# Performance work log

Measured on AMD Instinct MI355X. Metric: run time of the kernel, lower is better.

## Reference

```python
import jax, jax.numpy as jnp
from jax import lax
import numpy as np

IN_CH, OUT_CH, K, STRIDE = 4, 256, 16, 8
D_STATE, D_CONV, EXPAND, HEADDIM = 128, 4, 2, 64
D_INNER = EXPAND * OUT_CH            # 512
NHEADS = D_INNER // HEADDIM          # 8
CONV_DIM = D_INNER + 2 * D_STATE     # 768 (ngroups=1)
D_IN_PROJ = 2 * D_INNER + 2 * D_STATE + NHEADS  # 1288
B_SZ, L = 8, 16384


def _conv1d(x, w, b, stride, padding):
    y = lax.conv_general_dilated(x, w, (stride,), padding,
                                 dimension_numbers=('NCH', 'OIH', 'NCH'))
    return y + b[None, :, None]


def _mamba2(u, in_proj_w, conv1d_w, conv1d_b, dt_bias, A_log, D_skip, norm_w, out_proj_w):
    # u: (b, l, d_model). Faithful Mamba2 forward (ngroups=1, rmsnorm gated, no biases on projections).
    b, l, _ = u.shape
    zxbcdt = jnp.einsum('bld,ed->ble', u, in_proj_w)           # (b, l, d_in_proj)
    z = zxbcdt[..., :D_INNER]
    xBC = zxbcdt[..., D_INNER:D_INNER + CONV_DIM]
    dt = jax.nn.softplus(zxbcdt[..., D_INNER + CONV_DIM:] + dt_bias)  # (b, l, h)
    # causal depthwise conv (torch pads d_conv-1 both sides then truncates to :l == left-pad only) + SiLU
    xBC = lax.conv_general_dilated(xBC.transpose(0, 2, 1), conv1d_w, (1,),
                                   [(D_CONV - 1, 0)], feature_group_count=CONV_DIM,
                                   dimension_numbers=('NCH', 'OIH', 'NCH'))
    xBC = jax.nn.silu((xBC + conv1d_b[None, :, None]).transpose(0, 2, 1))  # (b, l, conv_dim)
    xs = xBC[..., :D_INNER].reshape(b, l, NHEADS, HEADDIM)
    Bm = xBC[..., D_INNER:D_INNER + D_STATE]                   # (b, l, n)
    Cm = xBC[..., D_INNER + D_STATE:]                          # (b, l, n)
    A = -jnp.exp(A_log)                                        # (h,), scalar A per head
    dA = jnp.exp(dt * A)                                       # (b, l, h)

    def step(h, inp):
        dA_t, dt_t, x_t, B_t, C_t = inp
        h = h * dA_t[:, :, None, None] + jnp.einsum('bh,bhp,bn->bhpn', dt_t, x_t, B_t)
        return h, jnp.einsum('bhpn,bn->bhp', h, C_t)

    h0 = jnp.zeros((b, NHEADS, HEADDIM, D_STATE), dtype=u.dtype)
    _, ys = lax.scan(step, h0, (dA.swapaxes(0, 1), dt.swapaxes(0, 1),
                                xs.swapaxes(0, 1), Bm.swapaxes(0, 1), Cm.swapaxes(0, 1)))
    y = ys.swapaxes(0, 1) + D_skip[None, None, :, None] * xs   # (b, l, h, p)
    y = y.reshape(b, l, D_INNER) * jax.nn.silu(z)              # gated RMSNorm (norm_before_gate=False)
    y = y * lax.rsqrt(jnp.mean(y * y, axis=-1, keepdims=True) + 1e-5) * norm_w
    return jnp.einsum('ble,de->bld', y, out_proj_w)


def _forward(x, conv_w, conv_b, in_proj_w, conv1d_w, conv1d_b, dt_bias, A_log,
             D_skip, norm_w, out_proj_w, conv1_w, conv1_b, convT_w, convT_b):
    h = jax.nn.relu(_conv1d(x, conv_w, conv_b, STRIDE, 'VALID'))       # (b, out_ch, l')
    y = _mamba2(h.transpose(0, 2, 1), in_proj_w, conv1d_w, conv1d_b,
                dt_bias, A_log, D_skip, norm_w, out_proj_w)
    y = y.transpose(0, 2, 1)                                           # (b, out_ch, l')
    y = _conv1d(y, conv1_w, conv1_b, 1, [(7, 8)])  # torch padding='same', even kernel: left=7, right=8
    # ConvTranspose1d: torch weight (Cin, Cout, K) -> flipped OIH kernel + lhs dilation
    kern = jnp.flip(convT_w, -1).transpose(1, 0, 2)
    y = lax.conv_general_dilated(y, kern, (1,), [(K - 1, K - 1)], lhs_dilation=(STRIDE,),
                                 dimension_numbers=('NCH', 'OIH', 'NCH'))
    return y + convT_b[None, :, None]


def setup_inputs() -> dict:
    key = jax.random.key(0)
    ks = jax.random.split(key, 16)
    n = lambda k, shp, sc=0.05: jax.random.normal(k, shp, dtype=jnp.float32) * sc
    return {
        'x': jax.random.normal(ks[0], (B_SZ, IN_CH, L), dtype=jnp.float32),
        'conv_w': n(ks[1], (OUT_CH, IN_CH, K)),
        'conv_b': n(ks[2], (OUT_CH,)),
        'in_proj_w': n(ks[3], (D_IN_PROJ, OUT_CH)),
        'conv1d_w': n(ks[4], (CONV_DIM, 1, D_CONV), 0.3),
        'conv1d_b': n(ks[5], (CONV_DIM,), 0.1),
        'dt_bias': n(ks[6], (NHEADS,), 0.5),
        'A_log': jnp.log(jax.random.uniform(ks[7], (NHEADS,), minval=1.0, maxval=16.0)),
        'D_skip': n(ks[8], (NHEADS,), 1.0),
        'norm_w': jnp.ones((D_INNER,), dtype=jnp.float32),
        'out_proj_w': n(ks[9], (OUT_CH, D_INNER)),
        'conv1_w': n(ks[10], (STRIDE, OUT_CH, K)),
        'conv1_b': n(ks[11], (STRIDE,)),
        'convT_w': n(ks[12], (STRIDE, IN_CH, K)),
        'convT_b': n(ks[13], (IN_CH,)),
    }


def reference(x, conv_w, conv_b, in_proj_w, conv1d_w, conv1d_b, dt_bias, A_log,
              D_skip, norm_w, out_proj_w, conv1_w, conv1_b, convT_w, convT_b):
    return _forward(x, conv_w, conv_b, in_proj_w, conv1d_w, conv1d_b, dt_bias, A_log,
                    D_skip, norm_w, out_proj_w, conv1_w, conv1_b, convT_w, convT_b)
```

## Files before the change

kernel.cpp:

```cpp
#include <hip/hip_runtime.h>
#include <cstddef>
#include <cstdint>

constexpr int L_IN   = 16384;
constexpr int L_SEQ  = 2047;
constexpr int BATCH  = 8;
constexpr int M_TOK  = BATCH * L_SEQ;
constexpr int D_INNER = 512;
constexpr int NHEADS  = 8;
constexpr int HEADDIM = 64;
constexpr int D_STATE = 128;
constexpr int CONV_DIM = 768;
constexpr int D_IN_PROJ = 1288;

constexpr int QC  = 64;
constexpr int NCH = 32;

constexpr int TP = 84;

constexpr size_t OFF_U    = 0;
constexpr size_t OFF_PB   = OFF_U   + 2096128;
constexpr size_t OFF_ZB   = OFF_U   + 4192256;
constexpr size_t OFF_XBC  = OFF_ZB  + 4192256;
constexpr size_t OFF_DT   = OFF_XBC + 6288384;
constexpr size_t OFF_AW   = OFF_DT  + 131008;
constexpr size_t OFF_XC   = OFF_AW  + 131008;
constexpr size_t OFF_Y    = OFF_XC  + 6288384;
constexpr size_t OFF_YC1  = OFF_Y   + 4192256;
constexpr size_t OFF_PBUF = OFF_YC1 + 131008;
constexpr size_t OFF_HS   = OFF_PBUF + 2048;
constexpr size_t OFF_WBIN = OFF_HS  + 8388608;
constexpr size_t OFF_WBF  = OFF_WBIN + 164864;
constexpr size_t OFF_W2   = OFF_WBF + 8192;

using short8 = __attribute__((ext_vector_type(8))) short;
using short4v = __attribute__((ext_vector_type(4))) short;
using f32x4  = __attribute__((ext_vector_type(4))) float;
typedef unsigned short ushort_t;

__device__ __forceinline__ ushort_t f2bf(float f) {
  uint32_t u = __float_as_uint(f);
  u += 0x7fffu + ((u >> 16) & 1u);
  return (ushort_t)(u >> 16);
}
__device__ __forceinline__ float bf2f(ushort_t h) {
  return __uint_as_float(((uint32_t)h) << 16);
}
__device__ __forceinline__ float siluf(float a) { return a / (1.f + expf(-a)); }
__device__ __forceinline__ short8 ld8(const short* p) {
  short4v a = *(const short4v*)p;
  short4v b = *(const short4v*)(p + 4);
  short8 r;
  r[0] = a[0]; r[1] = a[1]; r[2] = a[2]; r[3] = a[3];
  r[4] = b[0]; r[5] = b[1]; r[6] = b[2]; r[7] = b[3];
  return r;
}
#define MFMA16(a, b, c) __builtin_amdgcn_mfma_f32_16x16x32_bf16(a, b, c, 0, 0, 0)

#define GLD_LDS(gp, lp) __builtin_amdgcn_global_load_lds( \
    (const __attribute__((address_space(1))) void*)(gp),  \
    (__attribute__((address_space(3))) void*)(lp), 16, 0, 0)

__global__ __launch_bounds__(256) void k_prep(const float* __restrict__ x,
    const float* __restrict__ w1, const float* __restrict__ w3,
    const float* __restrict__ conv1_w, const float* __restrict__ wout,
    ushort_t* __restrict__ PB, ushort_t* __restrict__ o1, ushort_t* __restrict__ o3,
    ushort_t* __restrict__ W2b) {
  const int bid = blockIdx.x;
  const int tid = threadIdx.x;
  if (bid < 512) {
    int idx = bid * 256 + tid;
    if (idx >= M_TOK * 8) return;
    int oct = idx & 7, row = idx >> 3;
    int t = row % L_SEQ, b = row / L_SEQ;
    int ic = oct >> 1, k0 = (oct & 1) * 8;
    const float* src = x + ((size_t)b * 4 + ic) * L_IN + t * 8 + k0;
    float4 a0 = *(const float4*)src;
    float4 a1 = *(const float4*)(src + 4);
    short8 o;
    o[0] = (short)f2bf(a0.x); o[1] = (short)f2bf(a0.y);
    o[2] = (short)f2bf(a0.z); o[3] = (short)f2bf(a0.w);
    o[4] = (short)f2bf(a1.x); o[5] = (short)f2bf(a1.y);
    o[6] = (short)f2bf(a1.z); o[7] = (short)f2bf(a1.w);
    *(short8*)(PB + (size_t)row * 64 + oct * 8) = o;
  } else if (bid < 1800) {
    int i = (bid - 512) * 256 + tid;
    if (i < D_IN_PROJ * 256) o1[i] = f2bf(w1[i]);
    if (i < 256 * 64)        o3[i] = f2bf(w3[i]);
  } else {
    const int r = bid - 1800;
    const int oc = r >> 4, k = r & 15;
    const int d0 = tid;
    float acc0 = 0.f, acc1 = 0.f;
    for (int o = 0; o < 256; o++) {
      float wv = conv1_w[((size_t)oc * 256 + o) * 16 + k];
      acc0 = fmaf(wv, wout[(size_t)o * 512 + d0], acc0);
      acc1 = fmaf(wv, wout[(size_t)o * 512 + d0 + 256], acc1);
    }
    W2b[(size_t)r * 512 + d0]       = f2bf(acc0);
    W2b[(size_t)r * 512 + d0 + 256] = f2bf(acc1);
  }
}

template<int EPI>
__global__ __launch_bounds__(256) void gemm_bf16(const ushort_t* __restrict__ A, int lda,
    const ushort_t* __restrict__ B, int ldb, float* __restrict__ C,
    const float* __restrict__ bias, int M, int N, int K, int nx,
    ushort_t* __restrict__ zb, ushort_t* __restrict__ xbcb,
    float* __restrict__ dtb, float* __restrict__ awb,
    const float* __restrict__ dt_bias, const float* __restrict__ A_log) {
  __shared__ __attribute__((aligned(16))) ushort_t sA[2][128 * 64];
  __shared__ __attribute__((aligned(16))) ushort_t sB[2][128 * 64];
  const int tid = threadIdx.x;
  const int cpx = gridDim.x >> 3;
  const int swz = (blockIdx.x & 7) * cpx + (blockIdx.x >> 3);
  const int m0 = (swz / nx) * 128, n0 = (swz % nx) * 128;
  const int w = tid >> 6, lane = tid & 63;
  const int l15 = lane & 15, lK = lane >> 4;
  const int wr = w >> 1, wc = w & 1;
  f32x4 acc[4][4] = {};

  auto STAGE = [&](int buf, int k0) {
#pragma unroll
    for (int j = 0; j < 4; j++) {
      int idx = j * 256 + tid;
      int r = idx >> 3;
      int ss = (idx & 7) ^ (r & 7);
      GLD_LDS(A + (size_t)(m0 + r) * lda + k0 + ss * 8, &sA[buf][(j * 256 + w * 64) * 8]);
      GLD_LDS(B + (size_t)(n0 + r) * ldb + k0 + ss * 8, &sB[buf][(j * 256 + w * 64) * 8]);
    }
  };

  STAGE(0, 0);
  __syncthreads();
  int cur = 0;
  for (int k0 = 0; k0 < K; k0 += 64) {
    if (k0 + 64 < K) STAGE(cur ^ 1, k0 + 64);
#pragma unroll
    for (int kk = 0; kk < 2; kk++) {
      short8 af[4], bf[4];
#pragma unroll
      for (int mt = 0; mt < 4; mt++) {
        int r = wr * 64 + mt * 16 + l15;
        af[mt] = *(const short8*)&sA[cur][r * 64 + (((kk * 4 + lK) ^ (r & 7)) * 8)];
      }
#pragma unroll
      for (int nt = 0; nt < 4; nt++) {
        int r = wc * 64 + nt * 16 + l15;
        bf[nt] = *(const short8*)&sB[cur][r * 64 + (((kk * 4 + lK) ^ (r & 7)) * 8)];
      }
#pragma unroll
      for (int mt = 0; mt < 4; mt++)
#pragma unroll
        for (int nt = 0; nt < 4; nt++)
          acc[mt][nt] = MFMA16(af[mt], bf[nt], acc[mt][nt]);
    }
    __syncthreads();
    cur ^= 1;
  }
  if constexpr (EPI == 1) {
    ushort_t* Cb = (ushort_t*)C;
#pragma unroll
    for (int mt = 0; mt < 4; mt++)
#pragma unroll
      for (int i = 0; i < 4; i++) {
        int gm = m0 + wr * 64 + mt * 16 + lK * 4 + i;
#pragma unroll
        for (int nt = 0; nt < 4; nt++) {
          int gn = n0 + wc * 64 + nt * 16 + l15;
          float v = fmaxf(acc[mt][nt][i] + bias[gn], 0.f);
          uint32_t mine = f2bf(v);
          uint32_t other = (uint32_t)__shfl_xor((int)mine, 1, 64);
          if (((lane & 1) == 0) && gm < M)
            *(uint32_t*)(Cb + (size_t)gm * N + gn) = mine | (other << 16);
        }
      }
  } else if constexpr (EPI == 3) {
    ushort_t* Cb = (ushort_t*)C;
#pragma unroll
    for (int mt = 0; mt < 4; mt++)
#pragma unroll
      for (int i = 0; i < 4; i++) {
        int gm = m0 + wr * 64 + mt * 16 + lK * 4 + i;
#pragma unroll
        for (int nt = 0; nt < 4; nt++) {
          int gn = n0 + wc * 64 + nt * 16 + l15;
          uint32_t mine = f2bf(acc[mt][nt][i]);
          uint32_t other = (uint32_t)__shfl_xor((int)mine, 1, 64);
          if (((lane & 1) == 0) && gm < M)
            *(uint32_t*)(Cb + (size_t)gm * N + gn) = mine | (other << 16);
        }
      }
  } else {
    if (n0 < 1280) {
      ushort_t* dst = (n0 < 512) ? zb : xbcb;
      const int ldd  = (n0 < 512) ? 512 : 768;
      const int coff = (n0 < 512) ? 0 : 512;
#pragma unroll
      for (int mt = 0; mt < 4; mt++)
#pragma unroll
        for (int i = 0; i < 4; i++) {
          int gm = m0 + wr * 64 + mt * 16 + lK * 4 + i;
#pragma unroll
          for (int nt = 0; nt < 4; nt++) {
            int gn = n0 + wc * 64 + nt * 16 + l15;
            uint32_t mine = f2bf(acc[mt][nt][i]);
            uint32_t other = (uint32_t)__shfl_xor((int)mine, 1, 64);
            if (((lane & 1) == 0) && gm < M)
              *(uint32_t*)(dst + (size_t)gm * ldd + (gn - coff)) = mine | (other << 16);
          }
        }
    } else {
#pragma unroll
      for (int mt = 0; mt < 4; mt++)
#pragma unroll
        for (int i = 0; i < 4; i++) {
          int gm = m0 + wr * 64 + mt * 16 + lK * 4 + i;
          if (gm >= M) continue;
#pragma unroll
          for (int nt = 0; nt < 4; nt++) {
            int gn = n0 + wc * 64 + nt * 16 + l15;
            if (gn < N) {
              int hd = gn - 1280;
              float v = acc[mt][nt][i] + dt_bias[hd];
              float sp = (v > 20.f) ? v : log1pf(expf(v));
              dtb[(size_t)gm * 8 + hd] = sp;
              awb[(size_t)gm * 8 + hd] = -expf(A_log[hd]) * sp;
            }
          }
        }
    }
  }
}

__global__ __launch_bounds__(192) void k_dw(const ushort_t* __restrict__ xbcb,
    const float* __restrict__ w, const float* __restrict__ bias,
    ushort_t* __restrict__ xcb) {
  const int bid = blockIdx.x;
  const int tb = bid & 511, b = bid >> 9;
  const int t0 = tb * 4;
  const int c = threadIdx.x * 4;
  const size_t rowb = (size_t)b * L_SEQ;
  float wr[4][4];
#pragma unroll
  for (int j = 0; j < 4; j++)
#pragma unroll
    for (int k = 0; k < 4; k++) wr[j][k] = w[(c + j) * 4 + k];
  const float4 bs = {bias[c], bias[c + 1], bias[c + 2], bias[c + 3]};
  float v[7][4];
#pragma unroll
  for (int r = 0; r < 7; r++) {
    int tt = t0 - 3 + r;
    if (tt >= 0 && tt < L_SEQ) {
      uint2 pk = *(const uint2*)(xbcb + (rowb + tt) * CONV_DIM + c);
      v[r][0] = bf2f((ushort_t)(pk.x & 0xffff));
      v[r][1] = bf2f((ushort_t)(pk.x >> 16));
      v[r][2] = bf2f((ushort_t)(pk.y & 0xffff));
      v[r][3] = bf2f((ushort_t)(pk.y >> 16));
    } else {
      v[r][0] = v[r][1] = v[r][2] = v[r][3] = 0.f;
    }
  }
#pragma unroll
  for (int o = 0; o < 4; o++) {
    int t = t0 + o;
    if (t >= L_SEQ) break;
    float a0 = bs.x, a1 = bs.y, a2 = bs.z, a3 = bs.w;
#pragma unroll
    for (int k = 0; k < 4; k++) {
      a0 = fmaf(v[o + k][0], wr[0][k], a0);
      a1 = fmaf(v[o + k][1], wr[1][k], a1);
      a2 = fmaf(v[o + k][2], wr[2][k], a2);
      a3 = fmaf(v[o + k][3], wr[3][k], a3);
    }
    uint2 ov;
    ov.x = (uint32_t)f2bf(siluf(a0)) | ((uint32_t)f2bf(siluf(a1)) << 16);
    ov.y = (uint32_t)f2bf(siluf(a2)) | ((uint32_t)f2bf(siluf(a3)) << 16);
    *(uint2*)(xcb + (rowb + t) * CONV_DIM + c) = ov;
  }
}

__global__ __launch_bounds__(256) void k_ssd_state(const ushort_t* __restrict__ xcb,
    const float* __restrict__ dtb, const float* __restrict__ aw,
    ushort_t* __restrict__ HSb, float* __restrict__ Pbuf) {
  const int L = (blockIdx.x & 7) * 256 + (blockIdx.x >> 3);
  const int ch = L & 31, bh = L >> 5;
  const int b = bh >> 3, h = bh & 7;
  const int t0 = ch * QC;
  const int valid = (L_SEQ - t0 < QC) ? (L_SEQ - t0) : QC;
  const size_t rowbase = (size_t)b * L_SEQ;
  __shared__ __attribute__((aligned(16))) short sBT[128][TP];
  __shared__ __attribute__((aligned(16))) short sXw[64][TP];
  __shared__ float sW[64];
  __shared__ float sLtot;
  const int tid = threadIdx.x;
  if (tid < 64) {
    float aa = 0.f, dd = 0.f;
    if (tid < valid) { size_t r8 = (rowbase + t0 + tid) * 8 + h; aa = aw[r8]; dd = dtb[r8]; }
    float s = aa;
#pragma unroll
    for (int d = 1; d < 64; d <<= 1) { float o = __shfl_up(s, d, 64); if (tid >= d) s += o; }
    float Lt = __shfl(s, 63, 64);
    sW[tid] = expf(Lt - s) * dd;
    if (tid == 63) sLtot = s;
  }
  __syncthreads();
  for (int i = tid; i < 64 * 16; i += 256) {
    int r = i >> 4, q = (i & 15) * 8;
    short8 v = {0, 0, 0, 0, 0, 0, 0, 0};
    if (r < valid) v = *(const short8*)(xcb + (rowbase + t0 + r) * CONV_DIM + 512 + q);
#pragma unroll
    for (int j = 0; j < 8; j++) sBT[q + j][r] = v[j];
  }
  for (int i = tid; i < 64 * 8; i += 256) {
    int r = i >> 3, q = (i & 7) * 8;
    short8 v = {0, 0, 0, 0, 0, 0, 0, 0};
    if (r < valid) v = *(const short8*)(xcb + (rowbase + t0 + r) * CONV_DIM + h * 64 + q);
    float wv = sW[r];
#pragma unroll
    for (int j = 0; j < 8; j++) sXw[q + j][r] = (short)f2bf(bf2f((ushort_t)v[j]) * wv);
  }
  __syncthreads();
  const int w = tid >> 6, l15 = tid & 15, lK = (tid & 63) >> 4;
  f32x4 acc[2][4] = {};
  short8 afr[2][2];
#pragma unroll
  for (int j = 0; j < 2; j++)
#pragma unroll
    for (int kt = 0; kt < 2; kt++)
      afr[j][kt] = ld8(&sBT[(w * 2 + j) * 16 + l15][kt * 32 + lK * 8]);
#pragma unroll
  for (int pt = 0; pt < 4; pt++) {
#pragma unroll
    for (int kt = 0; kt < 2; kt++) {
      short8 bfr = ld8(&sXw[pt * 16 + l15][kt * 32 + lK * 8]);
      acc[0][pt] = MFMA16(afr[0][kt], bfr, acc[0][pt]);
      acc[1][pt] = MFMA16(afr[1][kt], bfr, acc[1][pt]);
    }
  }
  ushort_t* dst = HSb + ((size_t)bh * NCH + ch) * 8192;
#pragma unroll
  for (int j = 0; j < 2; j++)
#pragma unroll
    for (int pt = 0; pt < 4; pt++)
#pragma unroll
      for (int i = 0; i < 4; i++) {
        int n = (w * 2 + j) * 16 + lK * 4 + i, p = pt * 16 + l15;
        uint32_t mine = f2bf(acc[j][pt][i]);
        uint32_t other = (uint32_t)__shfl_xor((int)mine, 1, 64);
        if ((l15 & 1) == 0)
          *(uint32_t*)(dst + n * 64 + p) = mine | (other << 16);
      }
  if (tid == 0) Pbuf[bh * NCH + ch] = expf(sLtot);
}

__global__ __launch_bounds__(256) void k_ssd_comb(ushort_t* __restrict__ HSb,
                                                  const float* __restrict__ Pbuf) {
  const int bh = blockIdx.y;
  const int e2 = blockIdx.x * 256 + threadIdx.x;
  const size_t base = (size_t)bh * NCH * 8192 + (size_t)e2 * 2;
  uint32_t pk[NCH];
  float P[NCH];
#pragma unroll
  for (int c = 0; c < NCH; c++) pk[c] = *(const uint32_t*)(HSb + base + (size_t)c * 8192);
#pragma unroll
  for (int c = 0; c < NCH; c++) P[c] = Pbuf[bh * NCH + c];
  float run0 = 0.f, run1 = 0.f;
#pragma unroll
  for (int c = 0; c < NCH; c++) {
    run0 = fmaf(P[c], run0, bf2f((ushort_t)(pk[c] & 0xffff)));
    run1 = fmaf(P[c], run1, bf2f((ushort_t)(pk[c] >> 16)));
    pk[c] = (uint32_t)f2bf(run0) | ((uint32_t)f2bf(run1) << 16);
  }
#pragma unroll
  for (int c = 0; c < NCH; c++) *(uint32_t*)(HSb + base + (size_t)c * 8192) = pk[c];
}

__global__ __launch_bounds__(256) void k_ssd_y(const ushort_t* __restrict__ xcb,
    const float* __restrict__ dtb, const float* __restrict__ aw,
    const float* __restrict__ Dskip, const ushort_t* __restrict__ HSb,
    ushort_t* __restrict__ y16) {
  const int L = (blockIdx.x & 7) * 256 + (blockIdx.x >> 3);
  const int ch = L & 31, bh = L >> 5;
  const int b = bh >> 3, h = bh & 7;
  const int t0 = ch * QC;
  const int valid = (L_SEQ - t0 < QC) ? (L_SEQ - t0) : QC;
  const size_t rowbase = (size_t)b * L_SEQ;
  __shared__ __attribute__((aligned(16))) short sB[64][136];
  __shared__ __attribute__((aligned(16))) short sC[64][136];
  __shared__ __attribute__((aligned(16))) short sH[64][140];
  __shared__ __attribute__((aligned(16))) short sX[64][TP];
  __shared__ float sLrel[64], sdt[64], sEL[64];
  short (*sM)[72] = (short(*)[72])&sB[0][0];
  const int tid = threadIdx.x;
  if (tid < 64) {
    float aa = 0.f, dd = 0.f;
    if (tid < valid) { size_t r8 = (rowbase + t0 + tid) * 8 + h; aa = aw[r8]; dd = dtb[r8]; }
    float s = aa;
#pragma unroll
    for (int d = 1; d < 64; d <<= 1) { float o = __shfl_up(s, d, 64); if (tid >= d) s += o; }
    sLrel[tid] = s; sdt[tid] = dd; sEL[tid] = expf(s);
  }
  for (int i = tid; i < 64 * 16; i += 256) {
    int r = i >> 4, q = (i & 15) * 8;
    short8 vb = {0, 0, 0, 0, 0, 0, 0, 0}, vc = {0, 0, 0, 0, 0, 0, 0, 0};
    if (r < valid) {
      const ushort_t* rp = xcb + (rowbase + t0 + r) * CONV_DIM;
      vb = *(const short8*)(rp + 512 + q);
      vc = *(const short8*)(rp + 640 + q);
    }
    *(short8*)&sB[r][q] = vb;
    *(short8*)&sC[r][q] = vc;
  }
  for (int i = tid; i < 64 * 8; i += 256) {
    int r = i >> 3, q = (i & 7) * 8;
    short8 v = {0, 0, 0, 0, 0, 0, 0, 0};
    if (r < valid) v = *(const short8*)(xcb + (rowbase + t0 + r) * CONV_DIM + h * 64 + q);
#pragma unroll
    for (int j = 0; j < 8; j++) sX[q + j][r] = v[j];
  }
  for (int i = tid; i < 128 * 8; i += 256) {
    int n = i >> 3, q = (i & 7) * 8;
    short8 v = {0, 0, 0, 0, 0, 0, 0, 0};
    if (ch > 0) v = *(const short8*)(HSb + ((size_t)bh * NCH + (ch - 1)) * 8192 + n * 64 + q);
#pragma unroll
    for (int j = 0; j < 8; j++) sH[q + j][n] = v[j];
  }
  __syncthreads();
  const int w = tid >> 6, l15 = tid & 15, lK = (tid & 63) >> 4;
  short8 aC[4];
#pragma unroll
  for (int kt = 0; kt < 4; kt++)
    aC[kt] = *(const short8*)&sC[w * 16 + l15][kt * 32 + lK * 8];
  f32x4 g[4] = {};
#pragma unroll
  for (int st = 0; st < 4; st++)
#pragma unroll
    for (int kt = 0; kt < 4; kt++)
      g[st] = MFMA16(aC[kt], *(const short8*)&sB[st * 16 + l15][kt * 32 + lK * 8], g[st]);
  __syncthreads();
#pragma unroll
  for (int st = 0; st < 4; st++)
#pragma unroll
    for (int i = 0; i < 4; i++) {
      int tt = w * 16 + lK * 4 + i, ss = st * 16 + l15;
      float f = (ss <= tt) ? expf(sLrel[tt] - sLrel[ss]) * sdt[ss] : 0.f;
      sM[tt][ss] = (short)f2bf(g[st][i] * f);
    }
  __syncthreads();
  f32x4 acc[4] = {};
#pragma unroll
  for (int pt = 0; pt < 4; pt++)
#pragma unroll
    for (int kt = 0; kt < 4; kt++)
      acc[pt] = MFMA16(aC[kt], ld8(&sH[pt * 16 + l15][kt * 32 + lK * 8]), acc[pt]);
#pragma unroll
  for (int pt = 0; pt < 4; pt++)
#pragma unroll
    for (int i = 0; i < 4; i++)
      acc[pt][i] *= sEL[w * 16 + lK * 4 + i];
  short8 aM[2];
#pragma unroll
  for (int kt = 0; kt < 2; kt++)
    aM[kt] = *(const short8*)&sM[w * 16 + l15][kt * 32 + lK * 8];
#pragma unroll
  for (int pt = 0; pt < 4; pt++)
#pragma unroll
    for (int kt = 0; kt < 2; kt++)
      acc[pt] = MFMA16(aM[kt], ld8(&sX[pt * 16 + l15][kt * 32 + lK * 8]), acc[pt]);
  const float Dsk = Dskip[h];
#pragma unroll
  for (int pt = 0; pt < 4; pt++)
#pragma unroll
    for (int i = 0; i < 4; i++) {
      int tt = w * 16 + lK * 4 + i;
      int pp = pt * 16 + l15;
      float v = acc[pt][i] + Dsk * bf2f((ushort_t)sX[pp][tt]);
      uint32_t mine = f2bf(v);
      uint32_t other = (uint32_t)__shfl_xor((int)mine, 1, 64);
      if (((l15 & 1) == 0) && tt < valid)
        *(uint32_t*)(y16 + (rowbase + t0 + tt) * D_INNER + h * 64 + pp) = mine | (other << 16);
    }
}

__global__ __launch_bounds__(256) void k_norm(ushort_t* __restrict__ y16,
    const ushort_t* __restrict__ zb, const float* __restrict__ norm_w) {
  const int row = blockIdx.x * 4 + (threadIdx.x >> 6);
  const int lane = threadIdx.x & 63;
  const int c0 = lane * 8;
  ushort_t* yrow = y16 + (size_t)row * D_INNER;
  short8 yv = *(const short8*)(yrow + c0);
  short8 zv = *(const short8*)(zb + (size_t)row * 512 + c0);
  float v[8];
  float ss = 0.f;
#pragma unroll
  for (int j = 0; j < 8; j++) {
    float z = bf2f((ushort_t)zv[j]);
    float g = z / (1.f + expf(-z));
    v[j] = bf2f((ushort_t)yv[j]) * g;
    ss += v[j] * v[j];
  }
#pragma unroll
  for (int m = 32; m >= 1; m >>= 1) ss += __shfl_xor(ss, m, 64);
  float scale = rsqrtf(ss * (1.f / 512.f) + 1e-5f);
  float4 nw0 = *(const float4*)(norm_w + c0);
  float4 nw1 = *(const float4*)(norm_w + c0 + 4);
  short8 o;
  o[0] = (short)f2bf(v[0] * scale * nw0.x); o[1] = (short)f2bf(v[1] * scale * nw0.y);
  o[2] = (short)f2bf(v[2] * scale * nw0.z); o[3] = (short)f2bf(v[3] * scale * nw0.w);
  o[4] = (short)f2bf(v[4] * scale * nw1.x); o[5] = (short)f2bf(v[5] * scale * nw1.y);
  o[6] = (short)f2bf(v[6] * scale * nw1.z); o[7] = (short)f2bf(v[7] * scale * nw1.w);
  *(short8*)(yrow + c0) = o;
}

__global__ __launch_bounds__(256) void k_tail(const ushort_t* __restrict__ Yg,
    const float* __restrict__ b1, const float* __restrict__ wT,
    const float* __restrict__ bT, float* __restrict__ out) {
  const int bid = blockIdx.x;
  const int sc = bid & 31, b = bid >> 5;
  const int s0 = sc * 512;
  const int mbase = (s0 - 15) >> 3;
  const int tid = threadIdx.x;
  __shared__ float sY[8][66];
  __shared__ float swT[8][4][16];
  __shared__ float sb1[8], sbT[4];
  for (int i = tid; i < 512; i += 256) {
    int j = i >> 6, c = (i >> 4) & 3, k = i & 15;
    swT[j][c][k] = wT[((size_t)j * 4 + c) * 16 + k];
  }
  if (tid < 8) sb1[tid] = b1[tid];
  if (tid < 4) sbT[tid] = bT[tid];
  __syncthreads();
  const ushort_t* Yb = Yg + (size_t)b * L_SEQ * 128;
  for (int item = tid; item < 8 * 66; item += 256) {
    int j = item / 66, ii = item % 66;
    int m = mbase + ii;
    float acc = 0.f;
    if ((unsigned)m < (unsigned)L_SEQ) {
      acc = sb1[j];
#pragma unroll
      for (int k = 0; k < 16; k++) {
        int tt = m - 7 + k;
        if ((unsigned)tt < (unsigned)L_SEQ) acc += bf2f(Yb[(size_t)tt * 128 + j * 16 + k]);
      }
    }
    sY[j][ii] = acc;
  }
  __syncthreads();
  const int c = tid >> 6, si = tid & 63;
  float ov[8];
#pragma unroll
  for (int u = 0; u < 8; u++) {
    int s = s0 + si * 8 + u;
    float acc = sbT[c];
    const int k0 = (15 - u) & 7;
#pragma unroll
    for (int dk = 0; dk < 2; dk++) {
      int k = k0 + 8 * dk;
      int num = s - 15 + k;
      int m = num >> 3;
      if (num >= 0 && m < L_SEQ) {
        int ii = m - mbase;
#pragma unroll
        for (int j = 0; j < 8; j++)
          acc = fmaf(sY[j][ii], swT[j][c][15 - k], acc);
      }
    }
    ov[u] = acc;
  }
  float* op = out + ((size_t)b * 4 + c) * L_IN + s0 + si * 8;
  *(float4*)op       = *(float4*)&ov[0];
  *(float4*)(op + 4) = *(float4*)&ov[4];
}

extern "C" void kernel_launch(void* const* d_in, const int* in_sizes, int n_in,
                              void* d_out, int out_size, void* d_ws, size_t ws_size,
                              hipStream_t stream) {
  const float* x         = (const float*)d_in[0];
  const float* conv_w    = (const float*)d_in[1];
  const float* conv_b    = (const float*)d_in[2];
  const float* in_proj_w = (const float*)d_in[3];
  const float* conv1d_w  = (const float*)d_in[4];
  const float* conv1d_b  = (const float*)d_in[5];
  const float* dt_bias   = (const float*)d_in[6];
  const float* A_log     = (const float*)d_in[7];
  const float* D_skip    = (const float*)d_in[8];
  const float* norm_w    = (const float*)d_in[9];
  const float* out_proj_w= (const float*)d_in[10];
  const float* conv1_w   = (const float*)d_in[11];
  const float* conv1_b   = (const float*)d_in[12];
  const float* convT_w   = (const float*)d_in[13];
  const float* convT_b   = (const float*)d_in[14];
  float* out = (float*)d_out;
  float* ws  = (float*)d_ws;

  ushort_t* ub   = (ushort_t*)(ws + OFF_U);
  ushort_t* PB   = (ushort_t*)(ws + OFF_PB);
  ushort_t* zb   = (ushort_t*)(ws + OFF_ZB);
  ushort_t* xbcb = (ushort_t*)(ws + OFF_XBC);
  float* dtb  = ws + OFF_DT;
  float* awb  = ws + OFF_AW;
  ushort_t* xcb = (ushort_t*)(ws + OFF_XC);
  ushort_t* y16 = (ushort_t*)(ws + OFF_Y);
  float* Pbuf = ws + OFF_PBUF;
  ushort_t* HSb = (ushort_t*)(ws + OFF_HS);
  ushort_t* wbin  = (ushort_t*)(ws + OFF_WBIN);
  ushort_t* wbf   = (ushort_t*)(ws + OFF_WBF);
  ushort_t* W2b   = (ushort_t*)(ws + OFF_W2);
  ushort_t* Ygb = (ushort_t*)(ws + OFF_U);

  k_prep<<<dim3(1928), 256, 0, stream>>>(x, in_proj_w, conv_w, conv1_w, out_proj_w,
                                         PB, wbin, wbf, W2b);
  gemm_bf16<1><<<dim3(256), 256, 0, stream>>>(PB, 64, wbf, 64, (float*)ub,
      conv_b, M_TOK, 256, 64, 2, nullptr, nullptr, nullptr, nullptr, nullptr, nullptr);
  gemm_bf16<2><<<dim3(1408), 256, 0, stream>>>(ub, 256, wbin, 256, nullptr,
      nullptr, M_TOK, D_IN_PROJ, 256, 11, zb, xbcb, dtb, awb, dt_bias, A_log);
  k_dw<<<dim3(BATCH * 512), 192, 0, stream>>>(xbcb, conv1d_w, conv1d_b, xcb);
  k_ssd_state<<<dim3(2048), 256, 0, stream>>>(xcb, dtb, awb, HSb, Pbuf);
  k_ssd_comb<<<dim3(16, 64), 256, 0, stream>>>(HSb, Pbuf);
  k_ssd_y<<<dim3(2048), 256, 0, stream>>>(xcb, dtb, awb, D_skip, HSb, y16);
  k_norm<<<dim3(M_TOK / 4), 256, 0, stream>>>(y16, zb, norm_w);
  gemm_bf16<3><<<dim3(128), 256, 0, stream>>>(y16, 512, W2b, 512, (float*)Ygb,
      nullptr, M_TOK, 128, D_INNER, 1, nullptr, nullptr, nullptr, nullptr, nullptr, nullptr);
  k_tail<<<dim3(256), 256, 0, stream>>>(Ygb, conv1_b, convT_w, convT_b, out);
}
```

Baseline: 189.3 us.

## Fuse SiLU gate into SSD output and defer RMSNorm scale to GEMM epilogue

The SiLU(z) gating moves into the k_ssd_y epilogue, and the norm kernel now only computes a per-row rsqrt scale. That scale is applied in the final GEMM epilogue, with norm_w folded into the precomputed W2 weights. This drops the read-modify-write of y16 and the z read from the separate norm pass. In exchange, k_ssd_y does scattered, uncoalesced per-element z loads, and rounding order changes slightly because normalization is applied after the bf16 GEMM.

New measurement: 201.8 us. +6.6%, slower.

```diff
diff --git a/kernel.cpp b/kernel.cpp
--- a/kernel.cpp
+++ b/kernel.cpp
@@ -26,8 +26,8 @@
 constexpr size_t OFF_AW   = OFF_DT  + 131008;
 constexpr size_t OFF_XC   = OFF_AW  + 131008;
 constexpr size_t OFF_Y    = OFF_XC  + 6288384;
-constexpr size_t OFF_YC1  = OFF_Y   + 4192256;
-constexpr size_t OFF_PBUF = OFF_YC1 + 131008;
+constexpr size_t OFF_SCL  = OFF_Y   + 4192256;
+constexpr size_t OFF_PBUF = OFF_SCL + 131008;
 constexpr size_t OFF_HS   = OFF_PBUF + 2048;
 constexpr size_t OFF_WBIN = OFF_HS  + 8388608;
 constexpr size_t OFF_WBF  = OFF_WBIN + 164864;
@@ -64,6 +64,7 @@
 __global__ __launch_bounds__(256) void k_prep(const float* __restrict__ x,
     const float* __restrict__ w1, const float* __restrict__ w3,
     const float* __restrict__ conv1_w, const float* __restrict__ wout,
+    const float* __restrict__ norm_w,
     ushort_t* __restrict__ PB, ushort_t* __restrict__ o1, ushort_t* __restrict__ o3,
     ushort_t* __restrict__ W2b) {
   const int bid = blockIdx.x;
@@ -97,8 +98,8 @@
       acc0 = fmaf(wv, wout[(size_t)o * 512 + d0], acc0);
       acc1 = fmaf(wv, wout[(size_t)o * 512 + d0 + 256], acc1);
     }
-    W2b[(size_t)r * 512 + d0]       = f2bf(acc0);
-    W2b[(size_t)r * 512 + d0 + 256] = f2bf(acc1);
+    W2b[(size_t)r * 512 + d0]       = f2bf(acc0 * norm_w[d0]);
+    W2b[(size_t)r * 512 + d0 + 256] = f2bf(acc1 * norm_w[d0 + 256]);
   }
 }
 
@@ -182,10 +183,11 @@
 #pragma unroll
       for (int i = 0; i < 4; i++) {
         int gm = m0 + wr * 64 + mt * 16 + lK * 4 + i;
+        float sc = (gm < M) ? bias[gm] : 0.f;
 #pragma unroll
         for (int nt = 0; nt < 4; nt++) {
           int gn = n0 + wc * 64 + nt * 16 + l15;
-          uint32_t mine = f2bf(acc[mt][nt][i]);
+          uint32_t mine = f2bf(acc[mt][nt][i] * sc);
           uint32_t other = (uint32_t)__shfl_xor((int)mine, 1, 64);
           if (((lane & 1) == 0) && gm < M)
             *(uint32_t*)(Cb + (size_t)gm * N + gn) = mine | (other << 16);
@@ -377,6 +379,7 @@
 }
 
 __global__ __launch_bounds__(256) void k_ssd_y(const ushort_t* __restrict__ xcb,
+    const ushort_t* __restrict__ zb,
     const float* __restrict__ dtb, const float* __restrict__ aw,
     const float* __restrict__ Dskip, const ushort_t* __restrict__ HSb,
     ushort_t* __restrict__ y16) {
@@ -476,6 +479,10 @@
       int tt = w * 16 + lK * 4 + i;
       int pp = pt * 16 + l15;
       float v = acc[pt][i] + Dsk * bf2f((ushort_t)sX[pp][tt]);
+      if (tt < valid) {
+        float z = bf2f(zb[(rowbase + t0 + tt) * 512 + h * 64 + pp]);
+        v *= siluf(z);
+      }
       uint32_t mine = f2bf(v);
       uint32_t other = (uint32_t)__shfl_xor((int)mine, 1, 64);
       if (((l15 & 1) == 0) && tt < valid)
@@ -483,34 +490,22 @@
     }
 }
 
-__global__ __launch_bounds__(256) void k_norm(ushort_t* __restrict__ y16,
-    const ushort_t* __restrict__ zb, const float* __restrict__ norm_w) {
+__global__ __launch_bounds__(256) void k_scale(const ushort_t* __restrict__ y16,
+    float* __restrict__ scl) {
   const int row = blockIdx.x * 4 + (threadIdx.x >> 6);
   const int lane = threadIdx.x & 63;
   const int c0 = lane * 8;
-  ushort_t* yrow = y16 + (size_t)row * D_INNER;
-  short8 yv = *(const short8*)(yrow + c0);
-  short8 zv = *(const short8*)(zb + (size_t)row * 512 + c0);
-  float v[8];
+  short8 yv = *(const short8*)(y16 + (size_t)row * D_INNER + c0);
   float ss = 0.f;
 #pragma unroll
   for (int j = 0; j < 8; j++) {
-    float z = bf2f((ushort_t)zv[j]);
-    float g = z / (1.f + expf(-z));
-    v[j] = bf2f((ushort_t)yv[j]) * g;
-    ss += v[j] * v[j];
+    float v = bf2f((ushort_t)yv[j]);
+    ss += v * v;
   }
 #pragma unroll
   for (int m = 32; m >= 1; m >>= 1) ss += __shfl_xor(ss, m, 64);
-  float scale = rsqrtf(ss * (1.f / 512.f) + 1e-5f);
-  float4 nw0 = *(const float4*)(norm_w + c0);
-  float4 nw1 = *(const float4*)(norm_w + c0 + 4);
-  short8 o;
-  o[0] = (short)f2bf(v[0] * scale * nw0.x); o[1] = (short)f2bf(v[1] * scale * nw0.y);
-  o[2] = (short)f2bf(v[2] * scale * nw0.z); o[3] = (short)f2bf(v[3] * scale * nw0.w);
-  o[4] = (short)f2bf(v[4] * scale * nw1.x); o[5] = (short)f2bf(v[5] * scale * nw1.y);
-  o[6] = (short)f2bf(v[6] * scale * nw1.z); o[7] = (short)f2bf(v[7] * scale * nw1.w);
-  *(short8*)(yrow + c0) = o;
+  if (lane == 0)
+    scl[row] = rsqrtf(ss * (1.f / 512.f) + 1e-5f);
 }
 
 __global__ __launch_bounds__(256) void k_tail(const ushort_t* __restrict__ Yg,
@@ -602,6 +597,7 @@
   float* awb  = ws + OFF_AW;
   ushort_t* xcb = (ushort_t*)(ws + OFF_XC);
   ushort_t* y16 = (ushort_t*)(ws + OFF_Y);
+  float* scl  = ws + OFF_SCL;
   float* Pbuf = ws + OFF_PBUF;
   ushort_t* HSb = (ushort_t*)(ws + OFF_HS);
   ushort_t* wbin  = (ushort_t*)(ws + OFF_WBIN);
@@ -610,7 +606,7 @@
   ushort_t* Ygb = (ushort_t*)(ws + OFF_U);
 
   k_prep<<<dim3(1928), 256, 0, stream>>>(x, in_proj_w, conv_w, conv1_w, out_proj_w,
-                                         PB, wbin, wbf, W2b);
+                                         norm_w, PB, wbin, wbf, W2b);
   gemm_bf16<1><<<dim3(256), 256, 0, stream>>>(PB, 64, wbf, 64, (float*)ub,
       conv_b, M_TOK, 256, 64, 2, nullptr, nullptr, nullptr, nullptr, nullptr, nullptr);
   gemm_bf16<2><<<dim3(1408), 256, 0, stream>>>(ub, 256, wbin, 256, nullptr,
@@ -618,9 +614,9 @@
   k_dw<<<dim3(BATCH * 512), 192, 0, stream>>>(xbcb, conv1d_w, conv1d_b, xcb);
   k_ssd_state<<<dim3(2048), 256, 0, stream>>>(xcb, dtb, awb, HSb, Pbuf);
   k_ssd_comb<<<dim3(16, 64), 256, 0, stream>>>(HSb, Pbuf);
-  k_ssd_y<<<dim3(2048), 256, 0, stream>>>(xcb, dtb, awb, D_skip, HSb, y16);
-  k_norm<<<dim3(M_TOK / 4), 256, 0, stream>>>(y16, zb, norm_w);
+  k_ssd_y<<<dim3(2048), 256, 0, stream>>>(xcb, zb, dtb, awb, D_skip, HSb, y16);
+  k_scale<<<dim3(M_TOK / 4), 256, 0, stream>>>(y16, scl);
   gemm_bf16<3><<<dim3(128), 256, 0, stream>>>(y16, 512, W2b, 512, (float*)Ygb,
-      nullptr, M_TOK, 128, D_INNER, 1, nullptr, nullptr, nullptr, nullptr, nullptr, nullptr);
+      scl, M_TOK, 128, D_INNER, 1, nullptr, nullptr, nullptr, nullptr, nullptr, nullptr);
   k_tail<<<dim3(256), 256, 0, stream>>>(Ygb, conv1_b, convT_w, convT_b, out);
 }
```
